# Kernel optimization log

Measured on AMD Instinct MI355X. Metric: run time of the kernel, lower is better.

## Reference

```python
import jax, jax.numpy as jnp
import numpy as np
import math

N_KM = [64, 16]  # part_nums_hierarchical
SPATIAL = 891    # 11*9*9, hardcoded in the original reshape


def _make_im2cluster(C, K, seed):
    # random assignment but guarantee >=2 members per cluster (original code
    # indexes zs[0] and skips singleton clusters, but would crash on empties)
    rng = np.random.RandomState(seed)
    base = np.repeat(np.arange(K), 2)
    rest = rng.randint(0, K, size=C - base.size)
    return np.concatenate([base, rest]).astype(np.int64)


def setup_inputs() -> dict:
    key = jax.random.key(0)
    conv_features = jax.random.normal(key, (8, 4096, 11, 9, 9), dtype=jnp.float32)
    im2cluster_0 = jnp.asarray(_make_im2cluster(4096, 64, 1))
    im2cluster_1 = jnp.asarray(_make_im2cluster(4096, 16, 2))
    return {"conv_features": conv_features,
            "im2cluster_0": im2cluster_0,
            "im2cluster_1": im2cluster_1}


def _safe_norm(diff):
    # row-wise L2 norm, grad-safe at exactly-zero rows (row 0 is zs[0]-zs[0])
    sq = jnp.sum(diff * diff, axis=1)
    return jnp.where(sq > 0, jnp.sqrt(jnp.where(sq > 0, sq, 1.0)), 0.0)


def _hpro_loss(conv_features, im2clusters):
    bs, C = conv_features.shape[0], conv_features.shape[1]
    D = SPATIAL * bs
    x = conv_features.reshape(bs, C, SPATIAL)
    loss = jnp.float32(0.0)
    loss_node = jnp.float32(0.0)
    for m, K in enumerate(N_KM):
        im2c = np.asarray(im2clusters[m])  # constant indices -> concrete group sizes
        zs_m, conc_m = [], []
        for c in range(K):
            idx = np.nonzero(im2c == c)[0]
            # faithful torch reshape: [bs, n_c, 891] -> [n_c, 891*bs] (row-major)
            zs = x[:, idx, :].reshape(-1, D)
            n_c = zs.shape[0]
            norm_sum = jnp.sum(_safe_norm(zs - zs[0]))
            conc_m.append(norm_sum / (n_c * math.log(n_c + 10)))
            zs_m.append(zs)
        rs = jnp.stack([z[0] for z in zs_m], axis=1)  # [D, K] first-member reps
        for c in range(K):
            u1 = zs_m[c]
            if u1.shape[0] == 1:
                continue
            nom = jnp.sum(u1 * u1[0], axis=1) / conc_m[c]                     # [n_c]
            den = jax.scipy.special.logsumexp((u1 @ rs) / conc_m[c], axis=1)  # [n_c]
            loss = loss + (-(nom - den)).mean()
        if m == 0:
            loss_node = loss
    return loss_node / C, (loss - loss_node) / (len(N_KM) * C)


def reference(conv_features, im2cluster_0, im2cluster_1):
    return _hpro_loss(conv_features, [im2cluster_0, im2cluster_1])
```

## Files before the change

### kernel.cpp

```cpp
#include <hip/hip_runtime.h>
#include <math.h>

#define CCH 4096
#define SP 891
#define NSL 32768

typedef __attribute__((ext_vector_type(8))) short short8;
typedef __attribute__((ext_vector_type(4))) float f32x4;

__device__ __forceinline__ unsigned int pack_bf2(float a, float b) {
  unsigned int ua = __builtin_bit_cast(unsigned int, a);
  unsigned int ub = __builtin_bit_cast(unsigned int, b);
  ua = (ua + 0x7fffu + ((ua >> 16) & 1u)) >> 16;
  ub = (ub + 0x7fffu + ((ub >> 16) & 1u)) >> 16;
  return ua | (ub << 16);
}

__global__ void k_setup(const int* __restrict__ im0, const int* __restrict__ im1,
                        int* cnt0, int* off0, int* cnt1, int* off1,
                        int* mem0, int* mem1, int* rs0, int* rs1, int* inv1) {
  int cb = blockIdx.x;
  int level = (cb >= 64) ? 1 : 0;
  int c = level ? cb - 64 : cb;
  const int* im = level ? im1 : im0;
  int* members = level ? mem1 : mem0;
  int* rs = level ? rs1 : rs0;
  int lane = threadIdx.x;
  int lt = 0;
  for (int ch = lane; ch < CCH; ch += 64) lt += (im[ch] < c) ? 1 : 0;
  for (int o = 32; o; o >>= 1) lt += __shfl_xor(lt, o, 64);
  int base = lt;
  int cnt = 0;
  for (int chunk = 0; chunk < CCH; chunk += 64) {
    int ch = chunk + lane;
    bool m = (im[ch] == c);
    unsigned long long mk = __ballot(m);
    int pos = __popcll(mk & ((1ull << lane) - 1ull));
    if (m) members[base + cnt + pos] = ch;
    cnt += __popcll(mk);
  }
  int n = cnt;
  if (lane == 0) {
    if (level) { cnt1[c] = n; off1[c] = base; }
    else       { cnt0[c] = n; off0[c] = base; }
  }
  __syncthreads();
  for (int r = lane; r < n; r += 64) {
    #pragma unroll
    for (int q = 0; q < 8; q++) {
      int p = 8 * r + q;
      int b = p / n, j = p - b * n;
      int sid = b * CCH + members[base + j];
      rs[(size_t)(base + r) * 8 + q] = sid;
      if (level) inv1[sid] = ((base + r) << 3) | q;
    }
  }
}

__global__ void k_brep(const float* __restrict__ X,
    const int* __restrict__ off0, const int* __restrict__ off1,
    const int* __restrict__ rs0, const int* __restrict__ rs1,
    uint4* __restrict__ Bfrag0, uint4* __restrict__ Bfrag1) {
  int gid = blockIdx.x * 4 + (threadIdx.x >> 6);
  int l = threadIdx.x & 63;
  int lrow = l & 15, hi = l >> 4;
  int level = (gid >= 32) ? 1 : 0;
  int q = level ? (gid - 32) : (gid >> 2);
  int ct = level ? 0 : (gid & 3);
  int cc = ct * 16 + lrow;
  int base = level ? off1[cc] : off0[cc];
  int sid = (level ? rs1 : rs0)[(size_t)base * 8 + q];
  const float* ap = X + (size_t)sid * SP + hi * 8;
  uint4* dst = (level ? Bfrag1 + (size_t)(q * 28) * 64
                      : Bfrag0 + (size_t)((q * 4 + ct) * 28) * 64) + l;
  #pragma unroll 3
  for (int kc = 0; kc < 27; kc++) {
    float4 fa0 = *(const float4*)(ap + kc * 32);
    float4 fa1 = *(const float4*)(ap + kc * 32 + 4);
    uint4 ua;
    ua.x = pack_bf2(fa0.x, fa0.y); ua.y = pack_bf2(fa0.z, fa0.w);
    ua.z = pack_bf2(fa1.x, fa1.y); ua.w = pack_bf2(fa1.z, fa1.w);
    dst[kc * 64] = ua;
  }
  {
    float4 fa0, fa1;
    if (hi == 3) {
      fa0 = make_float4(ap[864], ap[865], ap[866], 0.f);
      fa1 = make_float4(0.f, 0.f, 0.f, 0.f);
    } else {
      fa0 = *(const float4*)(ap + 864);
      fa1 = *(const float4*)(ap + 868);
    }
    uint4 ua;
    ua.x = pack_bf2(fa0.x, fa0.y); ua.y = pack_bf2(fa0.z, fa0.w);
    ua.z = pack_bf2(fa1.x, fa1.y); ua.w = pack_bf2(fa1.z, fa1.w);
    dst[27 * 64] = ua;
  }
}

__global__ __launch_bounds__(256) void k_gemm0(const float* __restrict__ X,
    const int* __restrict__ rs0, const int* __restrict__ inv1,
    const uint4* __restrict__ Bfrag0, float* __restrict__ P8_0,
    unsigned short* __restrict__ Y1, float* __restrict__ sn2) {
  __shared__ __align__(16) unsigned short T[16 * 904];
  __shared__ int s_sid[16];
  const int rt = blockIdx.x, q = blockIdx.y, tid = threadIdx.x;
  const int l = tid & 63, w = tid >> 6;
  const int lrow = l & 15, hi = l >> 4;
  if (tid < 16) s_sid[tid] = rs0[(size_t)(rt * 16 + tid) * 8 + q];
  __syncthreads();
  const uint4* bq = Bfrag0 + (size_t)((q * 4 + w) * 28) * 64 + l;
  uint4 B0 = bq[0 * 64], B1 = bq[1 * 64], B2 = bq[2 * 64], B3 = bq[3 * 64];
  float4 sv[4][4];
  #pragma unroll
  for (int si = 0; si < 4; si++) {
    const float* sp = X + (size_t)s_sid[w * 4 + si] * SP;
    #pragma unroll
    for (int t = 0; t < 4; t++) {
      int el = t * 256 + 4 * l;
      float4 v;
      if (t < 3)           v = *(const float4*)(sp + el);
      else if (l <= 29)    v = *(const float4*)(sp + el);
      else if (l == 30)    v = make_float4(sp[888], sp[889], sp[890], 0.f);
      else                 v = make_float4(0.f, 0.f, 0.f, 0.f);
      sv[si][t] = v;
    }
  }
  #pragma unroll
  for (int si = 0; si < 4; si++) {
    int sid = s_sid[w * 4 + si];
    float s2 = 0.f;
    #pragma unroll
    for (int t = 0; t < 4; t++) {
      float4 v = sv[si][t];
      s2 += v.x * v.x + v.y * v.y + v.z * v.z + v.w * v.w;
    }
    for (int o = 32; o; o >>= 1) s2 += __shfl_xor(s2, o, 64);
    if (l == 0) sn2[sid] = s2;
    int inv = inv1[sid];
    unsigned short* y1 = Y1 + ((size_t)(inv & 7) * CCH + (inv >> 3)) * 896;
    unsigned short* Trow = T + (w * 4 + si) * 904;
    #pragma unroll
    for (int t = 0; t < 4; t++) {
      float4 v = sv[si][t];
      uint2 u;
      u.x = pack_bf2(v.x, v.y); u.y = pack_bf2(v.z, v.w);
      if (t < 3 || l < 32) {
        *(uint2*)(Trow + t * 256 + 4 * l) = u;
        *(uint2*)(y1 + t * 256 + 4 * l) = u;
      }
    }
  }
  __syncthreads();
  const char* Abase = (const char*)T + lrow * 1808;
  f32x4 acc = {0.f, 0.f, 0.f, 0.f};
  short8 A0 = *(const short8*)(Abase + (0 * 64 + hi * 16));
  short8 A1 = *(const short8*)(Abase + (1 * 64 + hi * 16));
  #pragma unroll
  for (int kc = 0; kc < 28; kc++) {
    short8 a = (kc & 1) ? A1 : A0;
    uint4 b = (kc & 3) == 0 ? B0 : (kc & 3) == 1 ? B1 : (kc & 3) == 2 ? B2 : B3;
    acc = __builtin_amdgcn_mfma_f32_16x16x32_bf16(a, __builtin_bit_cast(short8, b), acc, 0, 0, 0);
    if (kc + 2 < 28) {
      short8 an = *(const short8*)(Abase + ((kc + 2) * 64 + hi * 16));
      if (kc & 1) A1 = an; else A0 = an;
    }
    if (kc + 4 < 28) {
      uint4 bn = bq[(kc + 4) * 64];
      switch (kc & 3) { case 0: B0 = bn; break; case 1: B1 = bn; break;
                        case 2: B2 = bn; break; default: B3 = bn; }
    }
  }
  #pragma unroll
  for (int r = 0; r < 4; r++) {
    int row = rt * 16 + hi * 4 + r;
    P8_0[((size_t)q * CCH + row) * 64 + w * 16 + lrow] = acc[r];
  }
}

__global__ __launch_bounds__(256) void k_gemm1(const unsigned short* __restrict__ Y1,
    const uint4* __restrict__ Bfrag1, float* __restrict__ P8_1) {
  __shared__ __align__(16) unsigned short T[16 * 904];
  __shared__ float4 Rf[256];
  const int rt = blockIdx.x, q = blockIdx.y, tid = threadIdx.x;
  const int l = tid & 63, w = tid >> 6;
  const int lrow = l & 15, hi = l >> 4;
  const uint4* bq = Bfrag1 + (size_t)(q * 28) * 64 + l;
  #pragma unroll
  for (int si = 0; si < 4; si++) {
    int i = w * 4 + si;
    const unsigned short* src = Y1 + ((size_t)q * CCH + rt * 16 + i) * 896;
    uint4 a0 = *(const uint4*)(src + l * 8);
    uint4 a1 = (l < 48) ? *(const uint4*)(src + 512 + l * 8) : make_uint4(0, 0, 0, 0);
    *(uint4*)(T + i * 904 + l * 8) = a0;
    if (l < 48) *(uint4*)(T + i * 904 + 512 + l * 8) = a1;
  }
  __syncthreads();
  const char* Abase = (const char*)T + lrow * 1808;
  f32x4 acc = {0.f, 0.f, 0.f, 0.f};
  #pragma unroll
  for (int kk = 0; kk < 7; kk++) {
    int kc = w * 7 + kk;
    short8 a = *(const short8*)(Abase + (kc * 64 + hi * 16));
    uint4 b = bq[kc * 64];
    acc = __builtin_amdgcn_mfma_f32_16x16x32_bf16(a, __builtin_bit_cast(short8, b), acc, 0, 0, 0);
  }
  __syncthreads();
  Rf[w * 64 + l] = make_float4(acc[0], acc[1], acc[2], acc[3]);
  __syncthreads();
  if (w == 0) {
    float4 v0 = Rf[l], v1 = Rf[64 + l], v2 = Rf[128 + l], v3 = Rf[192 + l];
    float vr[4] = { v0.x + v1.x + v2.x + v3.x, v0.y + v1.y + v2.y + v3.y,
                    v0.z + v1.z + v2.z + v3.z, v0.w + v1.w + v2.w + v3.w };
    #pragma unroll
    for (int r = 0; r < 4; r++) {
      int row = rt * 16 + hi * 4 + r;
      P8_1[((size_t)q * CCH + row) * 16 + lrow] = vr[r];
    }
  }
}

template<int K>
__device__ __forceinline__ void fin_body(const float* __restrict__ P8,
    const float* __restrict__ sn2, const int* __restrict__ rs,
    const int* __restrict__ cnt, const int* __restrict__ off,
    double* __restrict__ clLoss, int c) {
  __shared__ float pcc[4096];
  __shared__ float red[512];
  __shared__ double redd[512];
  __shared__ float s_conc;
  const int n = cnt[c], base = off[c];
  const int tid = threadIdx.x;
  float rn0 = 0.f;
  #pragma unroll
  for (int qq = 0; qq < 8; qq++) rn0 += sn2[rs[(size_t)base * 8 + qq]];
  float t = 0.f;
  for (int r = tid; r < n; r += 512) {
    float pd = 0.f, rn = 0.f;
    #pragma unroll
    for (int qq = 0; qq < 8; qq++) {
      pd += P8[((size_t)qq * CCH + base + r) * K + c];
      rn += sn2[rs[(size_t)(base + r) * 8 + qq]];
    }
    pcc[r] = pd;
    if (r > 0) {
      float d2 = rn - 2.f * pd + rn0;
      t += (d2 > 0.f) ? sqrtf(d2) : 0.f;
    }
  }
  red[tid] = t; __syncthreads();
  for (int o = 256; o; o >>= 1) { if (tid < o) red[tid] += red[tid + o]; __syncthreads(); }
  if (tid == 0) s_conc = red[0] / ((float)n * logf((float)n + 10.f));
  __syncthreads();
  const float invc = 1.f / s_conc;
  const int wv = tid >> 6, lane = tid & 63;
  const int sub = (K == 64) ? 0 : (lane >> 4);
  const int cc = lane & (K - 1);
  constexpr int RPI = 8 * (64 / K);
  double acc = 0.0;
  for (int r = wv * (64 / K) + sub; r < n; r += RPI) {
    float s = 0.f;
    #pragma unroll
    for (int qq = 0; qq < 8; qq++) s += P8[((size_t)qq * CCH + base + r) * K + cc];
    float lg = s * invc;
    float m = lg;
    #pragma unroll
    for (int o = K / 2; o; o >>= 1) m = fmaxf(m, __shfl_xor(m, o, K));
    float e = expf(lg - m);
    float se = e;
    #pragma unroll
    for (int o = K / 2; o; o >>= 1) se += __shfl_xor(se, o, K);
    if (cc == 0) acc += (double)(m + logf(se)) - (double)(pcc[r] * invc);
  }
  redd[tid] = acc; __syncthreads();
  for (int o = 256; o; o >>= 1) { if (tid < o) redd[tid] += redd[tid + o]; __syncthreads(); }
  if (tid == 0) clLoss[c] = redd[0] / (double)n;
}

__global__ __launch_bounds__(512) void k_fin_all(const float* __restrict__ P8_0,
    const float* __restrict__ P8_1, const float* __restrict__ sn2,
    const int* __restrict__ rs0, const int* __restrict__ rs1,
    const int* __restrict__ cnt0, const int* __restrict__ off0,
    const int* __restrict__ cnt1, const int* __restrict__ off1,
    double* __restrict__ cl0, double* __restrict__ cl1) {
  if (blockIdx.x < 64) fin_body<64>(P8_0, sn2, rs0, cnt0, off0, cl0, blockIdx.x);
  else                 fin_body<16>(P8_1, sn2, rs1, cnt1, off1, cl1, blockIdx.x - 64);
}

__global__ void k_final(const double* __restrict__ cl0, const double* __restrict__ cl1,
                        float* __restrict__ out) {
  if (threadIdx.x == 0) {
    double s0 = 0.0, s1 = 0.0;
    for (int i = 0; i < 64; i++) s0 += cl0[i];
    for (int i = 0; i < 16; i++) s1 += cl1[i];
    out[0] = (float)(s0 / 4096.0);
    out[1] = (float)(s1 / 8192.0);
  }
}

extern "C" void kernel_launch(void* const* d_in, const int* in_sizes, int n_in,
                              void* d_out, int out_size, void* d_ws, size_t ws_size,
                              hipStream_t stream) {
  const float* X = (const float*)d_in[0];
  const int* im0 = (const int*)d_in[1];
  const int* im1 = (const int*)d_in[2];
  float* out = (float*)d_out;

  char* w = (char*)d_ws;
  auto alloc = [&](size_t bytes) -> char* {
    char* p = w; w += (bytes + 255) & ~(size_t)255; return p;
  };
  int*    cnt0  = (int*)alloc(64 * 4);
  int*    off0  = (int*)alloc(64 * 4);
  int*    cnt1  = (int*)alloc(16 * 4);
  int*    off1  = (int*)alloc(16 * 4);
  int*    mem0  = (int*)alloc((size_t)CCH * 4);
  int*    mem1  = (int*)alloc((size_t)CCH * 4);
  int*    rs0   = (int*)alloc((size_t)CCH * 8 * 4);
  int*    rs1   = (int*)alloc((size_t)CCH * 8 * 4);
  int*    inv1  = (int*)alloc((size_t)NSL * 4);
  float*  sn2   = (float*)alloc((size_t)NSL * 4);
  uint4*  Bfrag0 = (uint4*)alloc((size_t)32 * 28 * 64 * 16);
  uint4*  Bfrag1 = (uint4*)alloc((size_t)8 * 28 * 64 * 16);
  unsigned short* Y1 = (unsigned short*)alloc((size_t)8 * CCH * 896 * 2);
  float*  P8_0  = (float*)alloc((size_t)8 * CCH * 64 * 4);
  float*  P8_1  = (float*)alloc((size_t)8 * CCH * 16 * 4);
  double* cl0   = (double*)alloc(64 * 8);
  double* cl1   = (double*)alloc(16 * 8);

  k_setup<<<80, 64, 0, stream>>>(im0, im1, cnt0, off0, cnt1, off1, mem0, mem1, rs0, rs1, inv1);
  k_brep<<<10, 256, 0, stream>>>(X, off0, off1, rs0, rs1, Bfrag0, Bfrag1);
  k_gemm0<<<dim3(256, 8), 256, 0, stream>>>(X, rs0, inv1, Bfrag0, P8_0, Y1, sn2);
  k_gemm1<<<dim3(256, 8), 256, 0, stream>>>(Y1, Bfrag1, P8_1);
  k_fin_all<<<80, 512, 0, stream>>>(P8_0, P8_1, sn2, rs0, rs1, cnt0, off0, cnt1, off1, cl0, cl1);
  k_final<<<1, 64, 0, stream>>>(cl0, cl1, out);
}
```

Baseline: 105.2 us.

## Split fp32 gather into coalesced pack pass, merge both level GEMMs into one launch

Adds a streaming pack kernel that reads X sequentially by slice id, computes squared norms, and scatters bf16 rows into both level-0 and level-1 permuted layouts. The level-0 and level-1 GEMMs are then merged into one launch that reads pre-packed bf16 rows from these buffers. The intent is to replace the scattered fp32 gather inside GEMM0 with contiguous reads and to cut one kernel launch. In exchange it writes and re-reads an extra bf16 copy of the whole input (about 58 MB more traffic) and adds a workspace buffer.

```diff
diff --git a/kernel.cpp b/kernel.cpp
--- a/kernel.cpp
+++ b/kernel.cpp
@@ -18,13 +18,15 @@
 
 __global__ void k_setup(const int* __restrict__ im0, const int* __restrict__ im1,
                         int* cnt0, int* off0, int* cnt1, int* off1,
-                        int* mem0, int* mem1, int* rs0, int* rs1, int* inv1) {
+                        int* mem0, int* mem1, int* rs0, int* rs1,
+                        int* inv0, int* inv1) {
   int cb = blockIdx.x;
   int level = (cb >= 64) ? 1 : 0;
   int c = level ? cb - 64 : cb;
   const int* im = level ? im1 : im0;
   int* members = level ? mem1 : mem0;
   int* rs = level ? rs1 : rs0;
+  int* inv = level ? inv1 : inv0;
   int lane = threadIdx.x;
   int lt = 0;
   for (int ch = lane; ch < CCH; ch += 64) lt += (im[ch] < c) ? 1 : 0;
@@ -52,7 +54,7 @@
       int b = p / n, j = p - b * n;
       int sid = b * CCH + members[base + j];
       rs[(size_t)(base + r) * 8 + q] = sid;
-      if (level) inv1[sid] = ((base + r) << 3) | q;
+      inv[sid] = ((base + r) << 3) | q;
     }
   }
 }
@@ -98,98 +100,64 @@
   }
 }
 
-__global__ __launch_bounds__(256) void k_gemm0(const float* __restrict__ X,
-    const int* __restrict__ rs0, const int* __restrict__ inv1,
-    const uint4* __restrict__ Bfrag0, float* __restrict__ P8_0,
-    unsigned short* __restrict__ Y1, float* __restrict__ sn2) {
+__global__ __launch_bounds__(256) void k_pack2(const float* __restrict__ X,
+    const int* __restrict__ inv0, const int* __restrict__ inv1,
+    unsigned short* __restrict__ Y0, unsigned short* __restrict__ Y1,
+    float* __restrict__ sn2) {
+  const int w = threadIdx.x >> 6, l = threadIdx.x & 63;
+  for (int sid = blockIdx.x * 4 + w; sid < NSL; sid += gridDim.x * 4) {
+    const float* sp = X + (size_t)sid * SP;
+    float4 v0, v1, v2, v3;
+    {
+      int el = 4 * l;
+      v0 = *(const float4*)(sp + el);
+      v1 = *(const float4*)(sp + 256 + el);
+      v2 = *(const float4*)(sp + 512 + el);
+      if (l <= 29)      v3 = *(const float4*)(sp + 768 + el);
+      else if (l == 30) v3 = make_float4(sp[888], sp[889], sp[890], 0.f);
+      else              v3 = make_float4(0.f, 0.f, 0.f, 0.f);
+    }
+    float s2 = v0.x * v0.x + v0.y * v0.y + v0.z * v0.z + v0.w * v0.w
+             + v1.x * v1.x + v1.y * v1.y + v1.z * v1.z + v1.w * v1.w
+             + v2.x * v2.x + v2.y * v2.y + v2.z * v2.z + v2.w * v2.w
+             + v3.x * v3.x + v3.y * v3.y + v3.z * v3.z + v3.w * v3.w;
+    for (int o = 32; o; o >>= 1) s2 += __shfl_xor(s2, o, 64);
+    if (l == 0) sn2[sid] = s2;
+    uint2 u0, u1, u2, u3;
+    u0.x = pack_bf2(v0.x, v0.y); u0.y = pack_bf2(v0.z, v0.w);
+    u1.x = pack_bf2(v1.x, v1.y); u1.y = pack_bf2(v1.z, v1.w);
+    u2.x = pack_bf2(v2.x, v2.y); u2.y = pack_bf2(v2.z, v2.w);
+    u3.x = pack_bf2(v3.x, v3.y); u3.y = pack_bf2(v3.z, v3.w);
+    int i0 = inv0[sid], i1 = inv1[sid];
+    unsigned short* d0 = Y0 + ((size_t)(i0 & 7) * CCH + (i0 >> 3)) * 896 + 4 * l;
+    unsigned short* d1 = Y1 + ((size_t)(i1 & 7) * CCH + (i1 >> 3)) * 896 + 4 * l;
+    *(uint2*)(d0) = u0;
+    *(uint2*)(d0 + 256) = u1;
+    *(uint2*)(d0 + 512) = u2;
+    if (l < 32) *(uint2*)(d0 + 768) = u3;
+    *(uint2*)(d1) = u0;
+    *(uint2*)(d1 + 256) = u1;
+    *(uint2*)(d1 + 512) = u2;
+    if (l < 32) *(uint2*)(d1 + 768) = u3;
+  }
+}
+
+__global__ __launch_bounds__(256) void k_gemm_all(
+    const unsigned short* __restrict__ Y0, const unsigned short* __restrict__ Y1,
+    const uint4* __restrict__ Bfrag0, const uint4* __restrict__ Bfrag1,
+    float* __restrict__ P8_0, float* __restrict__ P8_1) {
   __shared__ __align__(16) unsigned short T[16 * 904];
-  __shared__ int s_sid[16];
-  const int rt = blockIdx.x, q = blockIdx.y, tid = threadIdx.x;
+  __shared__ float4 Rf[256];
+  const int q = blockIdx.y, tid = threadIdx.x;
+  const int lev = blockIdx.x >> 8;
+  const int rt = blockIdx.x & 255;
   const int l = tid & 63, w = tid >> 6;
   const int lrow = l & 15, hi = l >> 4;
-  if (tid < 16) s_sid[tid] = rs0[(size_t)(rt * 16 + tid) * 8 + q];
-  __syncthreads();
-  const uint4* bq = Bfrag0 + (size_t)((q * 4 + w) * 28) * 64 + l;
-  uint4 B0 = bq[0 * 64], B1 = bq[1 * 64], B2 = bq[2 * 64], B3 = bq[3 * 64];
-  float4 sv[4][4];
-  #pragma unroll
-  for (int si = 0; si < 4; si++) {
-    const float* sp = X + (size_t)s_sid[w * 4 + si] * SP;
-    #pragma unroll
-    for (int t = 0; t < 4; t++) {
-      int el = t * 256 + 4 * l;
-      float4 v;
-      if (t < 3)           v = *(const float4*)(sp + el);
-      else if (l <= 29)    v = *(const float4*)(sp + el);
-      else if (l == 30)    v = make_float4(sp[888], sp[889], sp[890], 0.f);
-      else                 v = make_float4(0.f, 0.f, 0.f, 0.f);
-      sv[si][t] = v;
-    }
-  }
-  #pragma unroll
-  for (int si = 0; si < 4; si++) {
-    int sid = s_sid[w * 4 + si];
-    float s2 = 0.f;
-    #pragma unroll
-    for (int t = 0; t < 4; t++) {
-      float4 v = sv[si][t];
-      s2 += v.x * v.x + v.y * v.y + v.z * v.z + v.w * v.w;
-    }
-    for (int o = 32; o; o >>= 1) s2 += __shfl_xor(s2, o, 64);
-    if (l == 0) sn2[sid] = s2;
-    int inv = inv1[sid];
-    unsigned short* y1 = Y1 + ((size_t)(inv & 7) * CCH + (inv >> 3)) * 896;
-    unsigned short* Trow = T + (w * 4 + si) * 904;
-    #pragma unroll
-    for (int t = 0; t < 4; t++) {
-      float4 v = sv[si][t];
-      uint2 u;
-      u.x = pack_bf2(v.x, v.y); u.y = pack_bf2(v.z, v.w);
-      if (t < 3 || l < 32) {
-        *(uint2*)(Trow + t * 256 + 4 * l) = u;
-        *(uint2*)(y1 + t * 256 + 4 * l) = u;
-      }
-    }
-  }
-  __syncthreads();
-  const char* Abase = (const char*)T + lrow * 1808;
-  f32x4 acc = {0.f, 0.f, 0.f, 0.f};
-  short8 A0 = *(const short8*)(Abase + (0 * 64 + hi * 16));
-  short8 A1 = *(const short8*)(Abase + (1 * 64 + hi * 16));
-  #pragma unroll
-  for (int kc = 0; kc < 28; kc++) {
-    short8 a = (kc & 1) ? A1 : A0;
-    uint4 b = (kc & 3) == 0 ? B0 : (kc & 3) == 1 ? B1 : (kc & 3) == 2 ? B2 : B3;
-    acc = __builtin_amdgcn_mfma_f32_16x16x32_bf16(a, __builtin_bit_cast(short8, b), acc, 0, 0, 0);
-    if (kc + 2 < 28) {
-      short8 an = *(const short8*)(Abase + ((kc + 2) * 64 + hi * 16));
-      if (kc & 1) A1 = an; else A0 = an;
-    }
-    if (kc + 4 < 28) {
-      uint4 bn = bq[(kc + 4) * 64];
-      switch (kc & 3) { case 0: B0 = bn; break; case 1: B1 = bn; break;
-                        case 2: B2 = bn; break; default: B3 = bn; }
-    }
-  }
-  #pragma unroll
-  for (int r = 0; r < 4; r++) {
-    int row = rt * 16 + hi * 4 + r;
-    P8_0[((size_t)q * CCH + row) * 64 + w * 16 + lrow] = acc[r];
-  }
-}
-
-__global__ __launch_bounds__(256) void k_gemm1(const unsigned short* __restrict__ Y1,
-    const uint4* __restrict__ Bfrag1, float* __restrict__ P8_1) {
-  __shared__ __align__(16) unsigned short T[16 * 904];
-  __shared__ float4 Rf[256];
-  const int rt = blockIdx.x, q = blockIdx.y, tid = threadIdx.x;
-  const int l = tid & 63, w = tid >> 6;
-  const int lrow = l & 15, hi = l >> 4;
-  const uint4* bq = Bfrag1 + (size_t)(q * 28) * 64 + l;
+  const unsigned short* Y = lev ? Y1 : Y0;
   #pragma unroll
   for (int si = 0; si < 4; si++) {
     int i = w * 4 + si;
-    const unsigned short* src = Y1 + ((size_t)q * CCH + rt * 16 + i) * 896;
+    const unsigned short* src = Y + ((size_t)q * CCH + rt * 16 + i) * 896;
     uint4 a0 = *(const uint4*)(src + l * 8);
     uint4 a1 = (l < 48) ? *(const uint4*)(src + 512 + l * 8) : make_uint4(0, 0, 0, 0);
     *(uint4*)(T + i * 904 + l * 8) = a0;
@@ -197,25 +165,54 @@
   }
   __syncthreads();
   const char* Abase = (const char*)T + lrow * 1808;
-  f32x4 acc = {0.f, 0.f, 0.f, 0.f};
-  #pragma unroll
-  for (int kk = 0; kk < 7; kk++) {
-    int kc = w * 7 + kk;
-    short8 a = *(const short8*)(Abase + (kc * 64 + hi * 16));
-    uint4 b = bq[kc * 64];
-    acc = __builtin_amdgcn_mfma_f32_16x16x32_bf16(a, __builtin_bit_cast(short8, b), acc, 0, 0, 0);
-  }
-  __syncthreads();
-  Rf[w * 64 + l] = make_float4(acc[0], acc[1], acc[2], acc[3]);
-  __syncthreads();
-  if (w == 0) {
-    float4 v0 = Rf[l], v1 = Rf[64 + l], v2 = Rf[128 + l], v3 = Rf[192 + l];
-    float vr[4] = { v0.x + v1.x + v2.x + v3.x, v0.y + v1.y + v2.y + v3.y,
-                    v0.z + v1.z + v2.z + v3.z, v0.w + v1.w + v2.w + v3.w };
+  if (!lev) {
+    const uint4* bq = Bfrag0 + (size_t)((q * 4 + w) * 28) * 64 + l;
+    f32x4 acc = {0.f, 0.f, 0.f, 0.f};
+    short8 A0 = *(const short8*)(Abase + (0 * 64 + hi * 16));
+    short8 A1 = *(const short8*)(Abase + (1 * 64 + hi * 16));
+    uint4 B0 = bq[0 * 64], B1 = bq[1 * 64], B2 = bq[2 * 64], B3 = bq[3 * 64];
+    #pragma unroll
+    for (int kc = 0; kc < 28; kc++) {
+      short8 a = (kc & 1) ? A1 : A0;
+      uint4 b = (kc & 3) == 0 ? B0 : (kc & 3) == 1 ? B1 : (kc & 3) == 2 ? B2 : B3;
+      acc = __builtin_amdgcn_mfma_f32_16x16x32_bf16(a, __builtin_bit_cast(short8, b), acc, 0, 0, 0);
+      if (kc + 2 < 28) {
+        short8 an = *(const short8*)(Abase + ((kc + 2) * 64 + hi * 16));
+        if (kc & 1) A1 = an; else A0 = an;
+      }
+      if (kc + 4 < 28) {
+        uint4 bn = bq[(kc + 4) * 64];
+        switch (kc & 3) { case 0: B0 = bn; break; case 1: B1 = bn; break;
+                          case 2: B2 = bn; break; default: B3 = bn; }
+      }
+    }
     #pragma unroll
     for (int r = 0; r < 4; r++) {
       int row = rt * 16 + hi * 4 + r;
-      P8_1[((size_t)q * CCH + row) * 16 + lrow] = vr[r];
+      P8_0[((size_t)q * CCH + row) * 64 + w * 16 + lrow] = acc[r];
+    }
+  } else {
+    const uint4* bq = Bfrag1 + (size_t)(q * 28) * 64 + l;
+    f32x4 acc = {0.f, 0.f, 0.f, 0.f};
+    #pragma unroll
+    for (int kk = 0; kk < 7; kk++) {
+      int kc = w * 7 + kk;
+      short8 a = *(const short8*)(Abase + (kc * 64 + hi * 16));
+      uint4 b = bq[kc * 64];
+      acc = __builtin_amdgcn_mfma_f32_16x16x32_bf16(a, __builtin_bit_cast(short8, b), acc, 0, 0, 0);
+    }
+    __syncthreads();
+    Rf[w * 64 + l] = make_float4(acc[0], acc[1], acc[2], acc[3]);
+    __syncthreads();
+    if (w == 0) {
+      float4 v0 = Rf[l], v1 = Rf[64 + l], v2 = Rf[128 + l], v3 = Rf[192 + l];
+      float vr[4] = { v0.x + v1.x + v2.x + v3.x, v0.y + v1.y + v2.y + v3.y,
+                      v0.z + v1.z + v2.z + v3.z, v0.w + v1.w + v2.w + v3.w };
+      #pragma unroll
+      for (int r = 0; r < 4; r++) {
+        int row = rt * 16 + hi * 4 + r;
+        P8_1[((size_t)q * CCH + row) * 16 + lrow] = vr[r];
+      }
     }
   }
 }
@@ -318,20 +315,23 @@
   int*    mem1  = (int*)alloc((size_t)CCH * 4);
   int*    rs0   = (int*)alloc((size_t)CCH * 8 * 4);
   int*    rs1   = (int*)alloc((size_t)CCH * 8 * 4);
+  int*    inv0  = (int*)alloc((size_t)NSL * 4);
   int*    inv1  = (int*)alloc((size_t)NSL * 4);
   float*  sn2   = (float*)alloc((size_t)NSL * 4);
   uint4*  Bfrag0 = (uint4*)alloc((size_t)32 * 28 * 64 * 16);
   uint4*  Bfrag1 = (uint4*)alloc((size_t)8 * 28 * 64 * 16);
+  unsigned short* Y0 = (unsigned short*)alloc((size_t)8 * CCH * 896 * 2);
   unsigned short* Y1 = (unsigned short*)alloc((size_t)8 * CCH * 896 * 2);
   float*  P8_0  = (float*)alloc((size_t)8 * CCH * 64 * 4);
   float*  P8_1  = (float*)alloc((size_t)8 * CCH * 16 * 4);
   double* cl0   = (double*)alloc(64 * 8);
   double* cl1   = (double*)alloc(16 * 8);
 
-  k_setup<<<80, 64, 0, stream>>>(im0, im1, cnt0, off0, cnt1, off1, mem0, mem1, rs0, rs1, inv1);
+  k_setup<<<80, 64, 0, stream>>>(im0, im1, cnt0, off0, cnt1, off1,
+                                 mem0, mem1, rs0, rs1, inv0, inv1);
   k_brep<<<10, 256, 0, stream>>>(X, off0, off1, rs0, rs1, Bfrag0, Bfrag1);
-  k_gemm0<<<dim3(256, 8), 256, 0, stream>>>(X, rs0, inv1, Bfrag0, P8_0, Y1, sn2);
-  k_gemm1<<<dim3(256, 8), 256, 0, stream>>>(Y1, Bfrag1, P8_1);
+  k_pack2<<<2048, 256, 0, stream>>>(X, inv0, inv1, Y0, Y1, sn2);
+  k_gemm_all<<<dim3(512, 8), 256, 0, stream>>>(Y0, Y1, Bfrag0, Bfrag1, P8_0, P8_1);
   k_fin_all<<<80, 512, 0, stream>>>(P8_0, P8_1, sn2, rs0, rs1, cnt0, off0, cnt1, off1, cl0, cl1);
   k_final<<<1, 64, 0, stream>>>(cl0, cl1, out);
 }
```

After: 123.5 us. 17.4% more time.

## Fuse level-1 GEMM into level-0 GEMM kernel, dropping bf16 Y1 intermediate

Applied to the files above, without the earlier changes.

Merges the two GEMM kernels. Each block now computes its tile against both the level-0 reps and all eight level-1 rep slices, then writes level-1 results only for the slice that matches each row's inverse mapping. This removes the write and re-read of the large bf16 Y1 buffer and one kernel launch. In exchange each wave issues three times as many MFMAs, most of the level-1 results are thrown away, and more registers are held for the extra B fragments.

```diff
diff --git a/kernel.cpp b/kernel.cpp
--- a/kernel.cpp
+++ b/kernel.cpp
@@ -98,19 +98,28 @@
   }
 }
 
-__global__ __launch_bounds__(256) void k_gemm0(const float* __restrict__ X,
+__global__ __launch_bounds__(256) void k_gemm_all(const float* __restrict__ X,
     const int* __restrict__ rs0, const int* __restrict__ inv1,
-    const uint4* __restrict__ Bfrag0, float* __restrict__ P8_0,
-    unsigned short* __restrict__ Y1, float* __restrict__ sn2) {
+    const uint4* __restrict__ Bfrag0, const uint4* __restrict__ Bfrag1,
+    float* __restrict__ P8_0, float* __restrict__ P8_1, float* __restrict__ sn2) {
   __shared__ __align__(16) unsigned short T[16 * 904];
   __shared__ int s_sid[16];
+  __shared__ int s_inv[16];
   const int rt = blockIdx.x, q = blockIdx.y, tid = threadIdx.x;
   const int l = tid & 63, w = tid >> 6;
   const int lrow = l & 15, hi = l >> 4;
-  if (tid < 16) s_sid[tid] = rs0[(size_t)(rt * 16 + tid) * 8 + q];
+  if (tid < 16) {
+    int sid = rs0[(size_t)(rt * 16 + tid) * 8 + q];
+    s_sid[tid] = sid;
+    s_inv[tid] = inv1[sid];
+  }
   __syncthreads();
-  const uint4* bq = Bfrag0 + (size_t)((q * 4 + w) * 28) * 64 + l;
-  uint4 B0 = bq[0 * 64], B1 = bq[1 * 64], B2 = bq[2 * 64], B3 = bq[3 * 64];
+  const uint4* bq0 = Bfrag0 + (size_t)((q * 4 + w) * 28) * 64 + l;
+  const uint4* bqa = Bfrag1 + (size_t)((w * 2) * 28) * 64 + l;
+  const uint4* bqb = Bfrag1 + (size_t)((w * 2 + 1) * 28) * 64 + l;
+  uint4 C0 = bq0[0 * 64], C1 = bq0[1 * 64], C2 = bq0[2 * 64], C3 = bq0[3 * 64];
+  uint4 D0 = bqa[0 * 64], D1 = bqa[1 * 64], D2 = bqa[2 * 64], D3 = bqa[3 * 64];
+  uint4 E0 = bqb[0 * 64], E1 = bqb[1 * 64], E2 = bqb[2 * 64], E3 = bqb[3 * 64];
   float4 sv[4][4];
   #pragma unroll
   for (int si = 0; si < 4; si++) {
@@ -137,86 +146,54 @@
     }
     for (int o = 32; o; o >>= 1) s2 += __shfl_xor(s2, o, 64);
     if (l == 0) sn2[sid] = s2;
-    int inv = inv1[sid];
-    unsigned short* y1 = Y1 + ((size_t)(inv & 7) * CCH + (inv >> 3)) * 896;
     unsigned short* Trow = T + (w * 4 + si) * 904;
     #pragma unroll
     for (int t = 0; t < 4; t++) {
       float4 v = sv[si][t];
       uint2 u;
       u.x = pack_bf2(v.x, v.y); u.y = pack_bf2(v.z, v.w);
-      if (t < 3 || l < 32) {
-        *(uint2*)(Trow + t * 256 + 4 * l) = u;
-        *(uint2*)(y1 + t * 256 + 4 * l) = u;
-      }
+      if (t < 3 || l < 32) *(uint2*)(Trow + t * 256 + 4 * l) = u;
     }
   }
   __syncthreads();
   const char* Abase = (const char*)T + lrow * 1808;
-  f32x4 acc = {0.f, 0.f, 0.f, 0.f};
+  f32x4 acc0 = {0.f, 0.f, 0.f, 0.f};
+  f32x4 accA = {0.f, 0.f, 0.f, 0.f};
+  f32x4 accB = {0.f, 0.f, 0.f, 0.f};
   short8 A0 = *(const short8*)(Abase + (0 * 64 + hi * 16));
   short8 A1 = *(const short8*)(Abase + (1 * 64 + hi * 16));
+#define BSTEP(BQ, B0, B1, B2, B3, ACC) { \
+    uint4 b_ = (kc & 3) == 0 ? B0 : (kc & 3) == 1 ? B1 : (kc & 3) == 2 ? B2 : B3; \
+    ACC = __builtin_amdgcn_mfma_f32_16x16x32_bf16(a, __builtin_bit_cast(short8, b_), ACC, 0, 0, 0); \
+    if (kc + 4 < 28) { \
+      uint4 bn_ = BQ[(kc + 4) * 64]; \
+      switch (kc & 3) { case 0: B0 = bn_; break; case 1: B1 = bn_; break; \
+                        case 2: B2 = bn_; break; default: B3 = bn_; } \
+    } }
   #pragma unroll
   for (int kc = 0; kc < 28; kc++) {
     short8 a = (kc & 1) ? A1 : A0;
-    uint4 b = (kc & 3) == 0 ? B0 : (kc & 3) == 1 ? B1 : (kc & 3) == 2 ? B2 : B3;
-    acc = __builtin_amdgcn_mfma_f32_16x16x32_bf16(a, __builtin_bit_cast(short8, b), acc, 0, 0, 0);
+    BSTEP(bq0, C0, C1, C2, C3, acc0)
+    BSTEP(bqa, D0, D1, D2, D3, accA)
+    BSTEP(bqb, E0, E1, E2, E3, accB)
     if (kc + 2 < 28) {
       short8 an = *(const short8*)(Abase + ((kc + 2) * 64 + hi * 16));
       if (kc & 1) A1 = an; else A0 = an;
     }
-    if (kc + 4 < 28) {
-      uint4 bn = bq[(kc + 4) * 64];
-      switch (kc & 3) { case 0: B0 = bn; break; case 1: B1 = bn; break;
-                        case 2: B2 = bn; break; default: B3 = bn; }
-    }
-  }
+  }
+#undef BSTEP
   #pragma unroll
   for (int r = 0; r < 4; r++) {
     int row = rt * 16 + hi * 4 + r;
-    P8_0[((size_t)q * CCH + row) * 64 + w * 16 + lrow] = acc[r];
-  }
-}
-
-__global__ __launch_bounds__(256) void k_gemm1(const unsigned short* __restrict__ Y1,
-    const uint4* __restrict__ Bfrag1, float* __restrict__ P8_1) {
-  __shared__ __align__(16) unsigned short T[16 * 904];
-  __shared__ float4 Rf[256];
-  const int rt = blockIdx.x, q = blockIdx.y, tid = threadIdx.x;
-  const int l = tid & 63, w = tid >> 6;
-  const int lrow = l & 15, hi = l >> 4;
-  const uint4* bq = Bfrag1 + (size_t)(q * 28) * 64 + l;
-  #pragma unroll
-  for (int si = 0; si < 4; si++) {
-    int i = w * 4 + si;
-    const unsigned short* src = Y1 + ((size_t)q * CCH + rt * 16 + i) * 896;
-    uint4 a0 = *(const uint4*)(src + l * 8);
-    uint4 a1 = (l < 48) ? *(const uint4*)(src + 512 + l * 8) : make_uint4(0, 0, 0, 0);
-    *(uint4*)(T + i * 904 + l * 8) = a0;
-    if (l < 48) *(uint4*)(T + i * 904 + 512 + l * 8) = a1;
-  }
-  __syncthreads();
-  const char* Abase = (const char*)T + lrow * 1808;
-  f32x4 acc = {0.f, 0.f, 0.f, 0.f};
-  #pragma unroll
-  for (int kk = 0; kk < 7; kk++) {
-    int kc = w * 7 + kk;
-    short8 a = *(const short8*)(Abase + (kc * 64 + hi * 16));
-    uint4 b = bq[kc * 64];
-    acc = __builtin_amdgcn_mfma_f32_16x16x32_bf16(a, __builtin_bit_cast(short8, b), acc, 0, 0, 0);
-  }
-  __syncthreads();
-  Rf[w * 64 + l] = make_float4(acc[0], acc[1], acc[2], acc[3]);
-  __syncthreads();
-  if (w == 0) {
-    float4 v0 = Rf[l], v1 = Rf[64 + l], v2 = Rf[128 + l], v3 = Rf[192 + l];
-    float vr[4] = { v0.x + v1.x + v2.x + v3.x, v0.y + v1.y + v2.y + v3.y,
-                    v0.z + v1.z + v2.z + v3.z, v0.w + v1.w + v2.w + v3.w };
-    #pragma unroll
-    for (int r = 0; r < 4; r++) {
-      int row = rt * 16 + hi * 4 + r;
-      P8_1[((size_t)q * CCH + row) * 16 + lrow] = vr[r];
-    }
+    P8_0[((size_t)q * CCH + row) * 64 + w * 16 + lrow] = acc0[r];
+  }
+  const int f0 = w * 2, f1 = w * 2 + 1;
+  #pragma unroll
+  for (int r = 0; r < 4; r++) {
+    int inv = s_inv[hi * 4 + r];
+    int q1 = inv & 7, row1 = inv >> 3;
+    if (q1 == f0)      P8_1[((size_t)q1 * CCH + row1) * 16 + lrow] = accA[r];
+    else if (q1 == f1) P8_1[((size_t)q1 * CCH + row1) * 16 + lrow] = accB[r];
   }
 }
 
@@ -322,16 +299,16 @@
   float*  sn2   = (float*)alloc((size_t)NSL * 4);
   uint4*  Bfrag0 = (uint4*)alloc((size_t)32 * 28 * 64 * 16);
   uint4*  Bfrag1 = (uint4*)alloc((size_t)8 * 28 * 64 * 16);
-  unsigned short* Y1 = (unsigned short*)alloc((size_t)8 * CCH * 896 * 2);
   float*  P8_0  = (float*)alloc((size_t)8 * CCH * 64 * 4);
   float*  P8_1  = (float*)alloc((size_t)8 * CCH * 16 * 4);
   double* cl0   = (double*)alloc(64 * 8);
   double* cl1   = (double*)alloc(16 * 8);
 
-  k_setup<<<80, 64, 0, stream>>>(im0, im1, cnt0, off0, cnt1, off1, mem0, mem1, rs0, rs1, inv1);
+  k_setup<<<80, 64, 0, stream>>>(im0, im1, cnt0, off0, cnt1, off1,
+                                 mem0, mem1, rs0, rs1, inv1);
   k_brep<<<10, 256, 0, stream>>>(X, off0, off1, rs0, rs1, Bfrag0, Bfrag1);
-  k_gemm0<<<dim3(256, 8), 256, 0, stream>>>(X, rs0, inv1, Bfrag0, P8_0, Y1, sn2);
-  k_gemm1<<<dim3(256, 8), 256, 0, stream>>>(Y1, Bfrag1, P8_1);
+  k_gemm_all<<<dim3(256, 8), 256, 0, stream>>>(X, rs0, inv1, Bfrag0, Bfrag1,
+                                               P8_0, P8_1, sn2);
   k_fin_all<<<80, 512, 0, stream>>>(P8_0, P8_1, sn2, rs0, rs1, cnt0, off0, cnt1, off1, cl0, cl1);
   k_final<<<1, 64, 0, stream>>>(cl0, cl1, out);
 }
```

New measurement: 102.0 us. -3.1%, faster.
